# Kernel optimization log

Hardware: AMD Instinct MI355X
Metric: run time of the kernel (lower is better)

The kernel has to match this reference:

```python
import jax, jax.numpy as jnp
import numpy as np

THRESHOLD = 20.0
CIRCLE_OFFSETS = [(0, -3), (1, -3), (2, -2), (3, -1), (3, 0), (3, 1), (2, 2), (1, 3),
                  (0, 3), (-1, 3), (-2, 2), (-3, 1), (-3, 0), (-3, -1), (-2, -2), (-1, -3)]


def setup_inputs() -> dict:
    key = jax.random.key(0)
    image = jax.random.uniform(key, (4, 1, 1080, 1920), dtype=jnp.float32) * 255.0
    return {"image": image}


def _detect_9_consecutive(bits_16):
    # bits_16: int32 (N, H, W). Build 24-bit circular buffer, test all 16 rotations
    # for 9 consecutive set bits (window == 511) using arithmetic-only ops.
    lower_8 = bits_16 % 256
    buffer_24 = bits_16 + lower_8 * 65536  # (N, H, W) int32
    divisors = (jnp.int32(2) ** jnp.arange(16, dtype=jnp.int32)).reshape(16, 1, 1, 1)
    shifted = (buffer_24[None] // divisors) % 512  # (16, N, H, W)
    return jnp.any(shifted == 511, axis=0)  # (N, H, W) bool


def reference(image):
    N, C, H, W = image.shape
    img = image.astype(jnp.float32)
    # Replicate-pad by 3 and gather the 16 Bresenham circle pixels via shifted slices.
    padded = jnp.pad(img[:, 0], ((0, 0), (3, 3), (3, 3)), mode='edge')  # (N, H+6, W+6)
    circle = jnp.stack(
        [padded[:, 3 + dy:3 + dy + H, 3 + dx:3 + dx + W] for dy, dx in CIRCLE_OFFSETS],
        axis=-1)  # (N, H, W, 16)
    center = img[:, 0][..., None]  # (N, H, W, 1)
    diff = circle - center
    powers = (jnp.int32(1) << jnp.arange(16, dtype=jnp.int32)).reshape(1, 1, 1, 16)
    dark_bits = ((diff >= THRESHOLD).astype(jnp.int32) * powers).sum(axis=-1)
    bright_bits = ((diff <= -THRESHOLD).astype(jnp.int32) * powers).sum(axis=-1)
    detected = _detect_9_consecutive(dark_bits) | _detect_9_consecutive(bright_bits)
    return detected.astype(jnp.float32)[:, None]  # (N, 1, H, W)
```

## Files before the change

kernel.cpp:

```cpp
#include <hip/hip_runtime.h>

#define IMG_H 1080
#define IMG_W 1920
#define TILE_W 128
#define TILE_H 8
#define GXB (IMG_W / TILE_W)
#define GYB (IMG_H / TILE_H)
#define BAND_H (TILE_H + 6)
#define BAND_W 136
#define BAND_W4 (BAND_W / 4)

__device__ __forceinline__ unsigned det9(unsigned m) {
    unsigned x = m | (m << 16);
    unsigned t = x & (x >> 1);
    t &= t >> 2;
    t &= t >> 4;
    t &= x >> 8;
    return t;
}

#define STEP_GE(m, sc, val, thr)                                          \
    asm("v_cmp_ge_f32 %1, %2, %3\n\tv_addc_co_u32 %0, %1, %0, %0, %1"     \
        : "+v"(m), "=s"(sc) : "v"(val), "v"(thr))
#define STEP_LE(m, sc, val, thr)                                          \
    asm("v_cmp_le_f32 %1, %2, %3\n\tv_addc_co_u32 %0, %1, %0, %0, %1"     \
        : "+v"(m), "=s"(sc) : "v"(val), "v"(thr))

__global__ __launch_bounds__(256) void fast_score_kernel(const float* __restrict__ img,
                                                         float* __restrict__ out) {
    __shared__ float band[BAND_H][BAND_W];

    int bid = blockIdx.x;
    {
        const int nwg = gridDim.x;
        const int q = nwg >> 3, r = nwg & 7;
        const int xcd = bid & 7, idx = bid >> 3;
        bid = (xcd < r ? xcd * (q + 1) : r * (q + 1) + (xcd - r) * q) + idx;
    }
    const int bx = bid % GXB;
    const int t0 = bid / GXB;
    const int by = t0 % GYB;
    const int n  = t0 / GYB;

    const int tx  = threadIdx.x;
    const int ty  = threadIdx.y;
    const int tid = ty * TILE_W + tx;

    const int gx0 = bx * TILE_W;
    const int y0  = by * TILE_H;

    const float* base = img + (size_t)n * (IMG_H * IMG_W);

    if (bx > 0 && bx < GXB - 1) {
#pragma unroll
        for (int i = tid; i < BAND_H * BAND_W4; i += 256) {
            const int r = i / BAND_W4;
            const int c = i - r * BAND_W4;
            const int ry = min(max(y0 - 3 + r, 0), IMG_H - 1);
            const float4 v =
                *(const float4*)(base + (size_t)ry * IMG_W + (gx0 - 4 + c * 4));
            *(float4*)&band[r][c * 4] = v;
        }
    } else {
        for (int i = tid; i < BAND_H * BAND_W; i += 256) {
            const int r  = i / BAND_W;
            const int c  = i - r * BAND_W;
            const int ry = min(max(y0 - 3 + r, 0), IMG_H - 1);
            const int cx = min(max(gx0 - 4 + c, 0), IMG_W - 1);
            band[r][c] = base[(size_t)ry * IMG_W + cx];
        }
    }
    __syncthreads();

    constexpr int DY[16] = {0, 1, 2, 3, 3, 3, 2, 1, 0, -1, -2, -3, -3, -3, -2, -1};
    constexpr int DX[16] = {-3, -3, -2, -1, 0, 1, 2, 3, 3, 3, 2, 1, 0, -1, -2, -3};

    const int cx = tx + 4;
    float* obase = out + (size_t)n * (IMG_H * IMG_W) + (size_t)y0 * IMG_W + gx0 + tx;

#pragma unroll
    for (int i = 0; i < 4; ++i) {
        const int j  = ty * 4 + i;
        const int rr = j + 3;

        const float center = band[rr][cx];
        const float hi = center + 20.0f;
        const float lo = center - 20.0f;

        float tv[16];
#pragma unroll
        for (int k = 0; k < 16; ++k) {
            tv[k] = band[rr + DY[k]][cx + DX[k]];
        }

        unsigned dark = 0u, bright = 0u;
        unsigned long long sc0, sc1;
#pragma unroll
        for (int k = 0; k < 16; ++k) {
            STEP_GE(dark,   sc0, tv[k], hi);
            STEP_LE(bright, sc1, tv[k], lo);
        }

        obase[(size_t)j * IMG_W] = (det9(dark) | det9(bright)) ? 1.0f : 0.0f;
    }
}

extern "C" void kernel_launch(void* const* d_in, const int* in_sizes, int n_in,
                              void* d_out, int out_size, void* d_ws, size_t ws_size,
                              hipStream_t stream) {
    const float* img = (const float*)d_in[0];
    float* out = (float*)d_out;
    const int n_img = in_sizes[0] / (IMG_H * IMG_W);
    dim3 grid(GXB * GYB * n_img, 1, 1);
    dim3 block(TILE_W, 2, 1);
    fast_score_kernel<<<grid, block, 0, stream>>>(img, out);
}
```

Baseline: 97.04 us.

## Transpose shared band and reuse per-thread register window across rows

Stores the halo band column-major in LDS with an odd pitch of 15. Each thread loads a 7x10 register window once and reuses it for its four output rows, so it no longer issues 16 LDS reads per pixel. The global load switches from float4 vectorized loads on interior tiles to scalar clamped loads for every tile, which may raise global load instruction count. Register pressure also grows with the window array.

```diff
diff --git a/kernel.cpp b/kernel.cpp
--- a/kernel.cpp
+++ b/kernel.cpp
@@ -6,9 +6,9 @@
 #define TILE_H 8
 #define GXB (IMG_W / TILE_W)
 #define GYB (IMG_H / TILE_H)
-#define BAND_H (TILE_H + 6)
+#define BAND_H 14
 #define BAND_W 136
-#define BAND_W4 (BAND_W / 4)
+#define BAND_P 15
 
 __device__ __forceinline__ unsigned det9(unsigned m) {
     unsigned x = m | (m << 16);
@@ -28,7 +28,7 @@
 
 __global__ __launch_bounds__(256) void fast_score_kernel(const float* __restrict__ img,
                                                          float* __restrict__ out) {
-    __shared__ float band[BAND_H][BAND_W];
+    __shared__ float bandT[BAND_W][BAND_P];
 
     int bid = blockIdx.x;
     {
@@ -51,57 +51,74 @@
 
     const float* base = img + (size_t)n * (IMG_H * IMG_W);
 
-    if (bx > 0 && bx < GXB - 1) {
-#pragma unroll
-        for (int i = tid; i < BAND_H * BAND_W4; i += 256) {
-            const int r = i / BAND_W4;
-            const int c = i - r * BAND_W4;
-            const int ry = min(max(y0 - 3 + r, 0), IMG_H - 1);
-            const float4 v =
-                *(const float4*)(base + (size_t)ry * IMG_W + (gx0 - 4 + c * 4));
-            *(float4*)&band[r][c * 4] = v;
-        }
-    } else {
-        for (int i = tid; i < BAND_H * BAND_W; i += 256) {
-            const int r  = i / BAND_W;
-            const int c  = i - r * BAND_W;
-            const int ry = min(max(y0 - 3 + r, 0), IMG_H - 1);
-            const int cx = min(max(gx0 - 4 + c, 0), IMG_W - 1);
-            band[r][c] = base[(size_t)ry * IMG_W + cx];
-        }
+    for (int i = tid; i < BAND_W * (BAND_H / 2); i += 256) {
+        const int rp = i / BAND_W;
+        const int c  = i - rp * BAND_W;
+        const int r0 = rp * 2;
+        const int cg  = min(max(gx0 - 4 + c, 0), IMG_W - 1);
+        const int ry0 = min(max(y0 - 3 + r0, 0), IMG_H - 1);
+        const int ry1 = min(max(y0 - 2 + r0, 0), IMG_H - 1);
+        const float v0 = base[(size_t)ry0 * IMG_W + cg];
+        const float v1 = base[(size_t)ry1 * IMG_W + cg];
+        bandT[c][r0]     = v0;
+        bandT[c][r0 + 1] = v1;
     }
     __syncthreads();
+
+    const int cx = tx + 4;
+    const int w0 = ty * 4;
+
+    const float* cm3 = &bandT[cx - 3][w0];
+    const float* cm2 = &bandT[cx - 2][w0];
+    const float* cm1 = &bandT[cx - 1][w0];
+    const float* cc0 = &bandT[cx    ][w0];
+    const float* cp1 = &bandT[cx + 1][w0];
+    const float* cp2 = &bandT[cx + 2][w0];
+    const float* cp3 = &bandT[cx + 3][w0];
+
+    float win[7][10];
+#pragma unroll
+    for (int r = 2; r <= 7; ++r) {
+        win[0][r] = cm3[r];
+        win[6][r] = cp3[r];
+    }
+#pragma unroll
+    for (int r = 1; r <= 8; ++r) {
+        win[1][r] = cm2[r];
+        win[5][r] = cp2[r];
+    }
+#pragma unroll
+    for (int r = 0; r <= 3; ++r) {
+        win[2][r]     = cm1[r];
+        win[4][r]     = cp1[r];
+        win[2][r + 6] = cm1[r + 6];
+        win[4][r + 6] = cp1[r + 6];
+    }
+#pragma unroll
+    for (int r = 0; r <= 9; ++r) {
+        win[3][r] = cc0[r];
+    }
 
     constexpr int DY[16] = {0, 1, 2, 3, 3, 3, 2, 1, 0, -1, -2, -3, -3, -3, -2, -1};
     constexpr int DX[16] = {-3, -3, -2, -1, 0, 1, 2, 3, 3, 3, 2, 1, 0, -1, -2, -3};
 
-    const int cx = tx + 4;
-    float* obase = out + (size_t)n * (IMG_H * IMG_W) + (size_t)y0 * IMG_W + gx0 + tx;
+    float* obase = out + ((size_t)n * IMG_H + y0 + w0) * IMG_W + gx0 + tx;
 
 #pragma unroll
-    for (int i = 0; i < 4; ++i) {
-        const int j  = ty * 4 + i;
-        const int rr = j + 3;
-
-        const float center = band[rr][cx];
+    for (int jj = 0; jj < 4; ++jj) {
+        const float center = win[3][jj + 3];
         const float hi = center + 20.0f;
         const float lo = center - 20.0f;
-
-        float tv[16];
-#pragma unroll
-        for (int k = 0; k < 16; ++k) {
-            tv[k] = band[rr + DY[k]][cx + DX[k]];
-        }
 
         unsigned dark = 0u, bright = 0u;
         unsigned long long sc0, sc1;
 #pragma unroll
         for (int k = 0; k < 16; ++k) {
-            STEP_GE(dark,   sc0, tv[k], hi);
-            STEP_LE(bright, sc1, tv[k], lo);
+            const float t = win[DX[k] + 3][jj + 3 + DY[k]];
+            STEP_GE(dark,   sc0, t, hi);
+            STEP_LE(bright, sc1, t, lo);
         }
-
-        obase[(size_t)j * IMG_W] = (det9(dark) | det9(bright)) ? 1.0f : 0.0f;
+        obase[(size_t)jj * IMG_W] = (det9(dark) | det9(bright)) ? 1.0f : 0.0f;
     }
 }
 
```

Result: no change. 97.68 us (+0.7%).

## Transpose shared band to column-major and compute six rows per thread

Applied to the files above, without the earlier changes.

Stores the halo band transposed so each thread reads whole columns with float4 LDS loads, then reuses each loaded column across six output rows per thread. The ring bits are built in two halves (A and B) that are reassembled with a bit reverse before the 9-consecutive test. This cuts LDS read traffic per output pixel. In exchange, global loads become scalar per column with clamping (no float4 fast path), the block shrinks to 128 threads, and register pressure rises.

```diff
diff --git a/kernel.cpp b/kernel.cpp
--- a/kernel.cpp
+++ b/kernel.cpp
@@ -3,12 +3,11 @@
 #define IMG_H 1080
 #define IMG_W 1920
 #define TILE_W 128
-#define TILE_H 8
+#define TILE_H 6
 #define GXB (IMG_W / TILE_W)
 #define GYB (IMG_H / TILE_H)
-#define BAND_H (TILE_H + 6)
 #define BAND_W 136
-#define BAND_W4 (BAND_W / 4)
+#define PITCH 12
 
 __device__ __forceinline__ unsigned det9(unsigned m) {
     unsigned x = m | (m << 16);
@@ -26,9 +25,33 @@
     asm("v_cmp_le_f32 %1, %2, %3\n\tv_addc_co_u32 %0, %1, %0, %0, %1"     \
         : "+v"(m), "=s"(sc) : "v"(val), "v"(thr))
 
-__global__ __launch_bounds__(256) void fast_score_kernel(const float* __restrict__ img,
+#define LOADCOL(CV, DXCOL)                                                \
+    {   const float4 q0 = *(const float4*)&bandT[cxb + (DXCOL)][0];       \
+        const float4 q1 = *(const float4*)&bandT[cxb + (DXCOL)][4];       \
+        const float4 q2 = *(const float4*)&bandT[cxb + (DXCOL)][8];       \
+        CV[0] = q0.x; CV[1] = q0.y; CV[2]  = q0.z; CV[3]  = q0.w;         \
+        CV[4] = q1.x; CV[5] = q1.y; CV[6]  = q1.z; CV[7]  = q1.w;         \
+        CV[8] = q2.x; CV[9] = q2.y; CV[10] = q2.z; CV[11] = q2.w; }
+
+#define ATAP(CV, RO)                                                      \
+    { STEP_GE(Ad[0], sc0, CV[0 + (RO)], hi[0]); STEP_LE(Ab[0], sc1, CV[0 + (RO)], lo[0]); \
+      STEP_GE(Ad[1], sc0, CV[1 + (RO)], hi[1]); STEP_LE(Ab[1], sc1, CV[1 + (RO)], lo[1]); \
+      STEP_GE(Ad[2], sc0, CV[2 + (RO)], hi[2]); STEP_LE(Ab[2], sc1, CV[2 + (RO)], lo[2]); \
+      STEP_GE(Ad[3], sc0, CV[3 + (RO)], hi[3]); STEP_LE(Ab[3], sc1, CV[3 + (RO)], lo[3]); \
+      STEP_GE(Ad[4], sc0, CV[4 + (RO)], hi[4]); STEP_LE(Ab[4], sc1, CV[4 + (RO)], lo[4]); \
+      STEP_GE(Ad[5], sc0, CV[5 + (RO)], hi[5]); STEP_LE(Ab[5], sc1, CV[5 + (RO)], lo[5]); }
+
+#define BTAP(CV, RO)                                                      \
+    { STEP_GE(Bd[0], sc0, CV[0 + (RO)], hi[0]); STEP_LE(Bb[0], sc1, CV[0 + (RO)], lo[0]); \
+      STEP_GE(Bd[1], sc0, CV[1 + (RO)], hi[1]); STEP_LE(Bb[1], sc1, CV[1 + (RO)], lo[1]); \
+      STEP_GE(Bd[2], sc0, CV[2 + (RO)], hi[2]); STEP_LE(Bb[2], sc1, CV[2 + (RO)], lo[2]); \
+      STEP_GE(Bd[3], sc0, CV[3 + (RO)], hi[3]); STEP_LE(Bb[3], sc1, CV[3 + (RO)], lo[3]); \
+      STEP_GE(Bd[4], sc0, CV[4 + (RO)], hi[4]); STEP_LE(Bb[4], sc1, CV[4 + (RO)], lo[4]); \
+      STEP_GE(Bd[5], sc0, CV[5 + (RO)], hi[5]); STEP_LE(Bb[5], sc1, CV[5 + (RO)], lo[5]); }
+
+__global__ __launch_bounds__(128) void fast_score_kernel(const float* __restrict__ img,
                                                          float* __restrict__ out) {
-    __shared__ float band[BAND_H][BAND_W];
+    __shared__ float bandT[BAND_W][PITCH];
 
     int bid = blockIdx.x;
     {
@@ -43,64 +66,60 @@
     const int n  = t0 / GYB;
 
     const int tx  = threadIdx.x;
-    const int ty  = threadIdx.y;
-    const int tid = ty * TILE_W + tx;
-
     const int gx0 = bx * TILE_W;
     const int y0  = by * TILE_H;
 
     const float* base = img + (size_t)n * (IMG_H * IMG_W);
 
-    if (bx > 0 && bx < GXB - 1) {
+    for (int c = tx; c < BAND_W; c += TILE_W) {
+        const int cg = min(max(gx0 - 4 + c, 0), IMG_W - 1);
+        float v[12];
 #pragma unroll
-        for (int i = tid; i < BAND_H * BAND_W4; i += 256) {
-            const int r = i / BAND_W4;
-            const int c = i - r * BAND_W4;
+        for (int r = 0; r < 12; ++r) {
             const int ry = min(max(y0 - 3 + r, 0), IMG_H - 1);
-            const float4 v =
-                *(const float4*)(base + (size_t)ry * IMG_W + (gx0 - 4 + c * 4));
-            *(float4*)&band[r][c * 4] = v;
+            v[r] = base[(size_t)ry * IMG_W + cg];
         }
-    } else {
-        for (int i = tid; i < BAND_H * BAND_W; i += 256) {
-            const int r  = i / BAND_W;
-            const int c  = i - r * BAND_W;
-            const int ry = min(max(y0 - 3 + r, 0), IMG_H - 1);
-            const int cx = min(max(gx0 - 4 + c, 0), IMG_W - 1);
-            band[r][c] = base[(size_t)ry * IMG_W + cx];
-        }
+        *(float4*)&bandT[c][0] = make_float4(v[0], v[1], v[2],  v[3]);
+        *(float4*)&bandT[c][4] = make_float4(v[4], v[5], v[6],  v[7]);
+        *(float4*)&bandT[c][8] = make_float4(v[8], v[9], v[10], v[11]);
     }
     __syncthreads();
 
-    constexpr int DY[16] = {0, 1, 2, 3, 3, 3, 2, 1, 0, -1, -2, -3, -3, -3, -2, -1};
-    constexpr int DX[16] = {-3, -3, -2, -1, 0, 1, 2, 3, 3, 3, 2, 1, 0, -1, -2, -3};
+    const int cxb = tx + 4;
 
-    const int cx = tx + 4;
-    float* obase = out + (size_t)n * (IMG_H * IMG_W) + (size_t)y0 * IMG_W + gx0 + tx;
+    float cv[12];
+    LOADCOL(cv, 0);
+    float hi[6], lo[6];
+#pragma unroll
+    for (int j = 0; j < 6; ++j) {
+        hi[j] = cv[j + 3] + 20.0f;
+        lo[j] = cv[j + 3] - 20.0f;
+    }
 
+    unsigned Ad[6] = {0, 0, 0, 0, 0, 0}, Ab[6] = {0, 0, 0, 0, 0, 0};
+    unsigned Bd[6] = {0, 0, 0, 0, 0, 0}, Bb[6] = {0, 0, 0, 0, 0, 0};
+    unsigned long long sc0, sc1;
+
+    LOADCOL(cv, -3);
+    ATAP(cv, 3); ATAP(cv, 4); BTAP(cv, 2);
+    LOADCOL(cv, -2);
+    ATAP(cv, 5); BTAP(cv, 1);
+    LOADCOL(cv, -1);
+    ATAP(cv, 6); BTAP(cv, 0);
+    LOADCOL(cv, 0);
+    ATAP(cv, 6); BTAP(cv, 0);
+    LOADCOL(cv, 1);
+    ATAP(cv, 6); BTAP(cv, 0);
+    LOADCOL(cv, 2);
+    ATAP(cv, 5); BTAP(cv, 1);
+    LOADCOL(cv, 3);
+    ATAP(cv, 4); BTAP(cv, 2); BTAP(cv, 3);
+
+    float* obase = out + ((size_t)n * IMG_H + y0) * IMG_W + gx0 + tx;
 #pragma unroll
-    for (int i = 0; i < 4; ++i) {
-        const int j  = ty * 4 + i;
-        const int rr = j + 3;
-
-        const float center = band[rr][cx];
-        const float hi = center + 20.0f;
-        const float lo = center - 20.0f;
-
-        float tv[16];
-#pragma unroll
-        for (int k = 0; k < 16; ++k) {
-            tv[k] = band[rr + DY[k]][cx + DX[k]];
-        }
-
-        unsigned dark = 0u, bright = 0u;
-        unsigned long long sc0, sc1;
-#pragma unroll
-        for (int k = 0; k < 16; ++k) {
-            STEP_GE(dark,   sc0, tv[k], hi);
-            STEP_LE(bright, sc1, tv[k], lo);
-        }
-
+    for (int j = 0; j < 6; ++j) {
+        const unsigned dark   = (Ad[j] << 8) | (__brev(Bd[j]) >> 24);
+        const unsigned bright = (Ab[j] << 8) | (__brev(Bb[j]) >> 24);
         obase[(size_t)j * IMG_W] = (det9(dark) | det9(bright)) ? 1.0f : 0.0f;
     }
 }
@@ -112,6 +131,6 @@
     float* out = (float*)d_out;
     const int n_img = in_sizes[0] / (IMG_H * IMG_W);
     dim3 grid(GXB * GYB * n_img, 1, 1);
-    dim3 block(TILE_W, 2, 1);
+    dim3 block(TILE_W, 1, 1);
     fast_score_kernel<<<grid, block, 0, stream>>>(img, out);
 }
```

After: 97.65 us. About the same (+0.6%).
